# Kernel optimization log

Hardware: AMD Instinct MI355X
Metric: run time of the kernel (lower is better)

## Reference

```python
import jax, jax.numpy as jnp
import numpy as np

BS, SEQ, D_SSL = 256, 201, 1024
D1, D2 = 128, 64
N_NODE = SEQ // 3          # 67 nodes after max_pool1d(3)
N_POOL = int(N_NODE * 0.8) # 53 nodes after GraphPool(k=0.8)
EPS = 1e-5                 # BatchNorm eps (eval mode, running stats)


def setup_inputs() -> dict:
    key = jax.random.key(0)
    ks = jax.random.split(key, 16)
    def rn(k, shape, s=0.02):
        return jax.random.normal(k, shape, jnp.float32) * s
    return {
        "feat": jax.random.normal(ks[0], (BS, SEQ, D_SSL), jnp.float32),
        "W_ll": rn(ks[1], (D_SSL, D1)), "b_ll": jnp.zeros((D1,), jnp.float32),
        "bn1_g": jnp.ones((D1,), jnp.float32), "bn1_b": jnp.zeros((D1,), jnp.float32),
        "bn1_m": rn(ks[2], (D1,), 0.1),
        "bn1_v": jax.random.uniform(ks[3], (D1,), jnp.float32, 0.5, 1.5),
        "W_ap": rn(ks[4], (D1, D2)), "b_ap": jnp.zeros((D2,), jnp.float32),
        "att_w": rn(ks[5], (D2, 1), 0.1),
        "W_pa": rn(ks[6], (D1, D2)), "b_pa": jnp.zeros((D2,), jnp.float32),
        "W_pn": rn(ks[7], (D1, D2)), "b_pn": jnp.zeros((D2,), jnp.float32),
        "bn2_g": jnp.ones((D2,), jnp.float32), "bn2_b": jnp.zeros((D2,), jnp.float32),
        "bn2_m": rn(ks[8], (D2,), 0.1),
        "bn2_v": jax.random.uniform(ks[9], (D2,), jnp.float32, 0.5, 1.5),
        "W_pool": rn(ks[10], (D2, 1), 0.1), "b_pool": jnp.zeros((1,), jnp.float32),
        "W_proj": rn(ks[11], (D2, 1), 0.1), "b_proj": jnp.zeros((1,), jnp.float32),
        "W_node": rn(ks[12], (N_POOL, 2), 0.1), "b_node": jnp.zeros((2,), jnp.float32),
    }


def _bn(x, g, b, m, v):
    # eval-mode BatchNorm1d with running stats, applied per-channel (last dim)
    return (x - m) * jax.lax.rsqrt(v + EPS) * g + b


def reference(feat, W_ll, b_ll, bn1_g, bn1_b, bn1_m, bn1_v,
              W_ap, b_ap, att_w, W_pa, b_pa, W_pn, b_pn,
              bn2_g, bn2_b, bn2_m, bn2_v,
              W_pool, b_pool, W_proj, b_proj, W_node, b_node):
    # LL: (bs, seq, 1024) -> (bs, seq, 128)
    x = feat @ W_ll + b_ll
    # max_pool1d(kernel=3, stride=3) over the sequence dim -> (bs, 67, 128)
    x = x[:, :N_NODE * 3].reshape(BS, N_NODE, 3, D1).max(axis=2)
    x = jax.nn.selu(_bn(x, bn1_g, bn1_b, bn1_m, bn1_v))
    # --- GraphAttentionLayer ---
    pair = x[:, :, None, :] * x[:, None, :, :]            # (bs, n, n, 128) pairwise mul
    att = jnp.tanh(pair @ W_ap + b_ap) @ att_w            # (bs, n, n, 1)
    att = jax.nn.softmax(att, axis=-2)                    # softmax over second node axis
    x1 = jnp.einsum('bij,bjd->bid', att[..., 0], x) @ W_pa + b_pa
    x2 = x @ W_pn + b_pn
    h = jax.nn.selu(_bn(x1 + x2, bn2_g, bn2_b, bn2_m, bn2_v))  # (bs, n, 64)
    # --- GraphPool: top-k node selection ---
    scores = jax.nn.sigmoid(h @ W_pool + b_pool)          # (bs, n, 1)
    _, idx = jax.lax.top_k(scores[..., 0], N_POOL)        # (bs, 53)
    hs = jnp.take_along_axis(h * scores, idx[:, :, None], axis=1)  # (bs, 53, 64)
    # head: proj -> (bs, 53), proj_node -> (bs, 2)
    out = (hs @ W_proj + b_proj)[..., 0] @ W_node + b_node
    return out
```

## Files before the change

### kernel.cpp

```cpp
#include <hip/hip_runtime.h>
#include <stdint.h>
#include <math.h>


#define BS 256
#define SEQ 201
#define DS 1024
#define D1 128
#define D2 64
#define NN 67
#define NP 53
#define ROWS1 (BS * SEQ)
#define ROWS2 (BS * NN)

#define SELU_LAM 1.0507009873554805f
#define SELU_ALP 1.6732632423543772f

__device__ __forceinline__ float selu_f(float x) {
    return (x > 0.0f) ? SELU_LAM * x : SELU_LAM * (SELU_ALP * expm1f(x));
}

__device__ __forceinline__ float fc(float4 v, int k) {
    switch (k & 3) {
        case 0: return v.x;
        case 1: return v.y;
        case 2: return v.z;
        default: return v.w;
    }
}

__global__ __launch_bounds__(256) void k_pre(
    const float* __restrict__ Wll, const float* __restrict__ Wap,
    const float* __restrict__ v1, const float* __restrict__ v2,
    float* __restrict__ WllT, float* __restrict__ WapT,
    float* __restrict__ r1, float* __restrict__ r2)
{
    int t = blockIdx.x * 256 + threadIdx.x;
    if (t < 131072) {
        int c = t >> 10, k = t & 1023;
        WllT[t] = Wll[k * D1 + c];
    } else if (t < 139264) {
        int i = t - 131072; int c = i >> 7, d = i & 127;
        WapT[i] = Wap[d * D2 + c];
    } else if (t < 139392) {
        int d = t - 139264;
        r1[d] = 1.0f / sqrtf(v1[d] + 1e-5f);
    } else if (t < 139456) {
        int c = t - 139392;
        r2[c] = 1.0f / sqrtf(v2[c] + 1e-5f);
    }
}

__global__ __launch_bounds__(256) void k_gemm1(
    const float* __restrict__ A, const float* __restrict__ Bt,
    float* __restrict__ y)
{
    __shared__ __align__(16) float As[128 * 36];
    __shared__ __align__(16) float Bs[128 * 36];
    int tid = threadIdx.x;
    int row0 = blockIdx.x * 128;
    int ty = tid >> 4, tx = tid & 15;
    float acc[8][8];
#pragma unroll
    for (int r = 0; r < 8; ++r)
#pragma unroll
        for (int m = 0; m < 8; ++m) acc[r][m] = 0.0f;

    int lr = tid >> 1, lc = (tid & 1) * 16;
    const float* gA = A + (size_t)(row0 + lr) * DS + lc;
    const float* gB = Bt + (size_t)lr * DS + lc;
    float* wa = As + lr * 36 + lc;
    float* wb = Bs + lr * 36 + lc;

    for (int k0 = 0; k0 < DS; k0 += 32) {
        float4 a0 = *(const float4*)(gA + k0);
        float4 a1 = *(const float4*)(gA + k0 + 4);
        float4 a2 = *(const float4*)(gA + k0 + 8);
        float4 a3 = *(const float4*)(gA + k0 + 12);
        float4 b0 = *(const float4*)(gB + k0);
        float4 b1 = *(const float4*)(gB + k0 + 4);
        float4 b2 = *(const float4*)(gB + k0 + 8);
        float4 b3 = *(const float4*)(gB + k0 + 12);
        __syncthreads();
        *(float4*)(wa)      = a0; *(float4*)(wa + 4)  = a1;
        *(float4*)(wa + 8)  = a2; *(float4*)(wa + 12) = a3;
        *(float4*)(wb)      = b0; *(float4*)(wb + 4)  = b1;
        *(float4*)(wb + 8)  = b2; *(float4*)(wb + 12) = b3;
        __syncthreads();
#pragma unroll
        for (int k4 = 0; k4 < 8; ++k4) {
            float4 av[8], bv[8];
#pragma unroll
            for (int r = 0; r < 8; ++r)
                av[r] = *(const float4*)(As + (ty + 16 * r) * 36 + k4 * 4);
#pragma unroll
            for (int m = 0; m < 8; ++m)
                bv[m] = *(const float4*)(Bs + (tx + 16 * m) * 36 + k4 * 4);
#pragma unroll
            for (int r = 0; r < 8; ++r)
#pragma unroll
                for (int m = 0; m < 8; ++m) {
                    acc[r][m] += av[r].x * bv[m].x;
                    acc[r][m] += av[r].y * bv[m].y;
                    acc[r][m] += av[r].z * bv[m].z;
                    acc[r][m] += av[r].w * bv[m].w;
                }
        }
    }
#pragma unroll
    for (int r = 0; r < 8; ++r)
#pragma unroll
        for (int m = 0; m < 8; ++m)
            y[(size_t)(row0 + ty + 16 * r) * D1 + tx + 16 * m] = acc[r][m];
}

__global__ __launch_bounds__(256) void k_pool(
    const float* __restrict__ y, const float* __restrict__ bll,
    const float* __restrict__ g1, const float* __restrict__ b1,
    const float* __restrict__ m1, const float* __restrict__ r1,
    float* __restrict__ X)
{
    int t = blockIdx.x * 256 + threadIdx.x;
    int d = t & 127, rem = t >> 7;
    int n = rem % NN, b = rem / NN;
    size_t base = ((size_t)(b * SEQ + 3 * n)) * D1 + d;
    float bl = bll[d];
    float v0 = y[base] + bl;
    float v1v = y[base + D1] + bl;
    float v2v = y[base + 2 * D1] + bl;
    float v = fmaxf(fmaxf(v0, v1v), v2v);
    v = (v - m1[d]) * r1[d] * g1[d] + b1[d];
    X[(size_t)rem * D1 + d] = selu_f(v);
}

__global__ __launch_bounds__(256) void k_attn1(
    const float* __restrict__ X, const float* __restrict__ WapT,
    const float* __restrict__ bap, const float* __restrict__ attw,
    float* __restrict__ epart)
{
    __shared__ __align__(16) float Xs[80 * 132];
    int tid = threadIdx.x;
    int blk = blockIdx.x;
    int b = blk >> 1, z = blk & 1;
    const float* Xb = X + (size_t)b * NN * D1;

#pragma unroll
    for (int q = 0; q < 40; ++q) {
        int t = q * 256 + tid;
        int r = t >> 7, d = t & 127;
        Xs[r * 132 + d] = (r < NN) ? Xb[(size_t)r * D1 + d] : 0.0f;
    }
    __syncthreads();

    int ti = tid >> 4, tj = tid & 15;

    float eacc[5][5];
#pragma unroll
    for (int a = 0; a < 5; ++a)
#pragma unroll
        for (int m = a; m < 5; ++m) eacc[a][m] = 0.0f;

    for (int cg = z * 8; cg < z * 8 + 8; ++cg) {
        float E[5][5][4];
#pragma unroll
        for (int a = 0; a < 5; ++a)
#pragma unroll
            for (int m = a; m < 5; ++m)
#pragma unroll
                for (int c = 0; c < 4; ++c) E[a][m][c] = 0.0f;

#pragma unroll 2
        for (int k4 = 0; k4 < 32; ++k4) {
            float4 xa[5], xv[5], w[4];
#pragma unroll
            for (int a = 0; a < 5; ++a)
                xa[a] = *(const float4*)(Xs + (ti + 16 * a) * 132 + k4 * 4);
#pragma unroll
            for (int m = 0; m < 5; ++m)
                xv[m] = *(const float4*)(Xs + (tj + 16 * m) * 132 + k4 * 4);
#pragma unroll
            for (int c = 0; c < 4; ++c)
                w[c] = *(const float4*)(WapT + (cg * 4 + c) * D1 + k4 * 4);
#pragma unroll
            for (int kk = 0; kk < 4; ++kk) {
#pragma unroll
                for (int a = 0; a < 5; ++a) {
                    float pa = fc(xa[a], kk);
#pragma unroll
                    for (int m = a; m < 5; ++m) {
                        float P = pa * fc(xv[m], kk);
                        E[a][m][0] += P * fc(w[0], kk);
                        E[a][m][1] += P * fc(w[1], kk);
                        E[a][m][2] += P * fc(w[2], kk);
                        E[a][m][3] += P * fc(w[3], kk);
                    }
                }
            }
        }
#pragma unroll
        for (int c = 0; c < 4; ++c) {
            float bc = bap[cg * 4 + c], ac = attw[cg * 4 + c];
#pragma unroll
            for (int a = 0; a < 5; ++a)
#pragma unroll
                for (int m = a; m < 5; ++m)
                    eacc[a][m] += tanhf(E[a][m][c] + bc) * ac;
        }
    }

    float* ep = epart + (size_t)blk * 6400;
#pragma unroll
    for (int a = 0; a < 5; ++a)
#pragma unroll
        for (int m = a; m < 5; ++m) {
            int i = ti + 16 * a, j = tj + 16 * m;
            ep[i * 80 + j] = eacc[a][m];
            if (a < m) ep[j * 80 + i] = eacc[a][m];
        }
}

__global__ __launch_bounds__(256) void k_attn2(
    const float* __restrict__ X, const float* __restrict__ epart,
    float* __restrict__ XA)
{
    __shared__ __align__(16) float Xs[80 * 132];
    __shared__ float e[80 * 85];
    int tid = threadIdx.x;
    int b = blockIdx.x;
    const float* Xb = X + (size_t)b * NN * D1;

#pragma unroll
    for (int q = 0; q < 40; ++q) {
        int t = q * 256 + tid;
        int r = t >> 7, d = t & 127;
        Xs[r * 132 + d] = (r < NN) ? Xb[(size_t)r * D1 + d] : 0.0f;
    }
    const float* e0 = epart + (size_t)(b * 2) * 6400;
    const float* e1 = e0 + 6400;
    for (int t = tid; t < 6400; t += 256) {
        int i = t / 80, j = t - i * 80;
        e[i * 85 + j] = e0[t] + e1[t];
    }
    __syncthreads();

    if (tid < NN) {
        float* er = e + tid * 85;
        float mx = -1e30f;
        for (int j = 0; j < NN; ++j) mx = fmaxf(mx, er[j]);
        float sum = 0.0f;
        for (int j = 0; j < NN; ++j) { float p = expf(er[j] - mx); er[j] = p; sum += p; }
        float inv = 1.0f / sum;
        for (int j = 0; j < NN; ++j) er[j] *= inv;
    }
    __syncthreads();

    int ti = tid >> 4, tj = tid & 15;
    int d0 = tj * 8;
    float o[5][8];
#pragma unroll
    for (int a = 0; a < 5; ++a)
#pragma unroll
        for (int dd = 0; dd < 8; ++dd) o[a][dd] = 0.0f;
    for (int j = 0; j < NN; ++j) {
        float4 x0 = *(const float4*)(Xs + j * 132 + d0);
        float4 x1 = *(const float4*)(Xs + j * 132 + d0 + 4);
        float av[5];
#pragma unroll
        for (int a = 0; a < 5; ++a) av[a] = e[(ti + 16 * a) * 85 + j];
#pragma unroll
        for (int a = 0; a < 5; ++a) {
            o[a][0] += av[a] * x0.x; o[a][1] += av[a] * x0.y;
            o[a][2] += av[a] * x0.z; o[a][3] += av[a] * x0.w;
            o[a][4] += av[a] * x1.x; o[a][5] += av[a] * x1.y;
            o[a][6] += av[a] * x1.z; o[a][7] += av[a] * x1.w;
        }
    }
#pragma unroll
    for (int a = 0; a < 5; ++a) {
        int i = ti + 16 * a;
        if (i < NN) {
            float* dst = XA + (size_t)(b * NN + i) * D1 + d0;
            float4 s0, s1;
            s0.x = o[a][0]; s0.y = o[a][1]; s0.z = o[a][2]; s0.w = o[a][3];
            s1.x = o[a][4]; s1.y = o[a][5]; s1.z = o[a][6]; s1.w = o[a][7];
            *(float4*)(dst) = s0;
            *(float4*)(dst + 4) = s1;
        }
    }
}

__global__ __launch_bounds__(256) void k_gemm2(
    const float* __restrict__ XAg, const float* __restrict__ Xg,
    const float* __restrict__ Wpa, const float* __restrict__ Wpn,
    const float* __restrict__ bpa, const float* __restrict__ bpn,
    const float* __restrict__ g2, const float* __restrict__ b2,
    const float* __restrict__ m2, const float* __restrict__ r2,
    float* __restrict__ h)
{
    __shared__ __align__(16) float As[64 * 260];
    __shared__ __align__(16) float Ws[256 * 68];
    int tid = threadIdx.x;
    int row0 = blockIdx.x * 64;
#pragma unroll
    for (int q = 0; q < 16; ++q) {
        int e4 = q * 256 + tid;
        int r = e4 >> 6, k4 = (e4 & 63) * 4;
        float4 v;
        if (k4 < 128) v = *(const float4*)(XAg + (size_t)(row0 + r) * D1 + k4);
        else          v = *(const float4*)(Xg + (size_t)(row0 + r) * D1 + (k4 - 128));
        *(float4*)(As + r * 260 + k4) = v;
    }
#pragma unroll
    for (int q = 0; q < 16; ++q) {
        int e4 = q * 256 + tid;
        int k = e4 >> 4, c4 = (e4 & 15) * 4;
        float4 v;
        if (k < 128) v = *(const float4*)(Wpa + k * D2 + c4);
        else         v = *(const float4*)(Wpn + (k - 128) * D2 + c4);
        *(float4*)(Ws + k * 68 + c4) = v;
    }
    __syncthreads();
    int rl = tid >> 2, cq = (tid & 3) * 16;
    float acc[16];
#pragma unroll
    for (int m = 0; m < 16; ++m) acc[m] = 0.0f;
    for (int k = 0; k < 256; ++k) {
        float a = As[rl * 260 + k];
        float4 w0 = *(const float4*)(Ws + k * 68 + cq);
        float4 w1 = *(const float4*)(Ws + k * 68 + cq + 4);
        float4 w2 = *(const float4*)(Ws + k * 68 + cq + 8);
        float4 w3 = *(const float4*)(Ws + k * 68 + cq + 12);
        acc[0] += a * w0.x;  acc[1] += a * w0.y;  acc[2] += a * w0.z;  acc[3] += a * w0.w;
        acc[4] += a * w1.x;  acc[5] += a * w1.y;  acc[6] += a * w1.z;  acc[7] += a * w1.w;
        acc[8] += a * w2.x;  acc[9] += a * w2.y;  acc[10] += a * w2.z; acc[11] += a * w2.w;
        acc[12] += a * w3.x; acc[13] += a * w3.y; acc[14] += a * w3.z; acc[15] += a * w3.w;
    }
#pragma unroll
    for (int m = 0; m < 16; ++m) {
        int c = cq + m;
        float t = acc[m] + bpa[c] + bpn[c];
        t = (t - m2[c]) * r2[c] * g2[c] + b2[c];
        h[(size_t)(row0 + rl) * D2 + c] = selu_f(t);
    }
}

__global__ __launch_bounds__(64) void k_head(
    const float* __restrict__ h, const float* __restrict__ Wpool,
    const float* __restrict__ bpool, const float* __restrict__ Wproj,
    const float* __restrict__ bproj, const float* __restrict__ Wnode,
    const float* __restrict__ bnode, float* __restrict__ out)
{
    __shared__ float sc[NN], pv[NN], sel[NP];
    int lane = threadIdx.x, b = blockIdx.x;
    for (int j = lane; j < NN; j += 64) {
        const float* hr = h + (size_t)(b * NN + j) * D2;
        float z = 0.0f;
        for (int c = 0; c < D2; ++c) z += hr[c] * Wpool[c];
        z += bpool[0];
        float s = 1.0f / (1.0f + expf(-z));
        float q = 0.0f;
        for (int c = 0; c < D2; ++c) q += (hr[c] * s) * Wproj[c];
        q += bproj[0];
        sc[j] = s; pv[j] = q;
    }
    __syncthreads();
    for (int j = lane; j < NN; j += 64) {
        float sj = sc[j]; int rank = 0;
        for (int k = 0; k < NN; ++k) {
            float sk = sc[k];
            rank += (sk > sj) || (sk == sj && k < j);
        }
        if (rank < NP) sel[rank] = pv[j];
    }
    __syncthreads();
    if (lane < 2) {
        float o = 0.0f;
        for (int r = 0; r < NP; ++r) o += sel[r] * Wnode[r * 2 + lane];
        out[b * 2 + lane] = o + bnode[lane];
    }
}

extern "C" void kernel_launch(void* const* d_in, const int* in_sizes, int n_in,
                              void* d_out, int out_size, void* d_ws, size_t ws_size,
                              hipStream_t stream)
{
    const float* feat  = (const float*)d_in[0];
    const float* Wll   = (const float*)d_in[1];
    const float* bll   = (const float*)d_in[2];
    const float* g1    = (const float*)d_in[3];
    const float* b1    = (const float*)d_in[4];
    const float* m1    = (const float*)d_in[5];
    const float* v1    = (const float*)d_in[6];
    const float* Wap   = (const float*)d_in[7];
    const float* bap   = (const float*)d_in[8];
    const float* attw  = (const float*)d_in[9];
    const float* Wpa   = (const float*)d_in[10];
    const float* bpa   = (const float*)d_in[11];
    const float* Wpn   = (const float*)d_in[12];
    const float* bpn   = (const float*)d_in[13];
    const float* g2    = (const float*)d_in[14];
    const float* b2    = (const float*)d_in[15];
    const float* m2    = (const float*)d_in[16];
    const float* v2    = (const float*)d_in[17];
    const float* Wpool = (const float*)d_in[18];
    const float* bpool = (const float*)d_in[19];
    const float* Wproj = (const float*)d_in[20];
    const float* bproj = (const float*)d_in[21];
    const float* Wnode = (const float*)d_in[22];
    const float* bnode = (const float*)d_in[23];
    float* out = (float*)d_out;

    char* w = (char*)d_ws;
    float* y    = (float*)w; w += (size_t)ROWS1 * D1 * 4;
    float* X    = (float*)w; w += (size_t)ROWS2 * D1 * 4;
    float* XA   = (float*)w; w += (size_t)ROWS2 * D1 * 4;
    float* hbuf = (float*)w; w += (size_t)ROWS2 * D2 * 4;
    float* WllT = (float*)w; w += (size_t)128 * 1024 * 4;
    float* WapT = (float*)w; w += (size_t)64 * 128 * 4;
    float* r1   = (float*)w; w += 128 * 4;
    float* r2   = (float*)w; w += 64 * 4;
    float* epart = y;

    hipLaunchKernelGGL(k_pre,   dim3(545),  dim3(256), 0, stream,
                       Wll, Wap, v1, v2, WllT, WapT, r1, r2);
    hipLaunchKernelGGL(k_gemm1, dim3(402),  dim3(256), 0, stream, feat, WllT, y);
    hipLaunchKernelGGL(k_pool,  dim3(8576), dim3(256), 0, stream,
                       y, bll, g1, b1, m1, r1, X);
    hipLaunchKernelGGL(k_attn1, dim3(512),  dim3(256), 0, stream,
                       X, WapT, bap, attw, epart);
    hipLaunchKernelGGL(k_attn2, dim3(256),  dim3(256), 0, stream,
                       X, epart, XA);
    hipLaunchKernelGGL(k_gemm2, dim3(268),  dim3(256), 0, stream,
                       XA, X, Wpa, Wpn, bpa, bpn, g2, b2, m2, r2, hbuf);
    hipLaunchKernelGGL(k_head,  dim3(256),  dim3(64),  0, stream,
                       hbuf, Wpool, bpool, Wproj, bproj, Wnode, bnode, out);
}
```

Measured before the change: 810.8 us.

## Split-K the input GEMM, prefetch A tiles, split attention further, stage head in LDS

The first GEMM now splits its K dimension in two across twice as many blocks, writing two partial outputs that the pooling kernel sums, and register-prefetches the next A tile while the current one is computed. The attention score kernel splits its channel groups four ways instead of two, and the softmax kernel sums four partials. The head kernel stages each batch's h rows into padded shared memory before its dot products. These aim to fill more of the GPU's compute units in the launch-bound 402- and 512-block grids, at the cost of an extra partial-output buffer that must be written and read back, and extra register pressure from the prefetch.

```diff
diff --git a/kernel.cpp b/kernel.cpp
--- a/kernel.cpp
+++ b/kernel.cpp
@@ -53,12 +53,22 @@
 
 __global__ __launch_bounds__(256) void k_gemm1(
     const float* __restrict__ A, const float* __restrict__ Bt,
-    float* __restrict__ y)
+    float* __restrict__ y0, float* __restrict__ y1, int nsplit)
 {
     __shared__ __align__(16) float As[128 * 36];
     __shared__ __align__(16) float Bs[128 * 36];
     int tid = threadIdx.x;
-    int row0 = blockIdx.x * 128;
+    int bx = blockIdx.x;
+    int tile, kb, nk;
+    float* yout;
+    if (nsplit == 2) {
+        tile = bx >> 1; int half = bx & 1;
+        kb = half << 9; nk = 512;
+        yout = half ? y1 : y0;
+    } else {
+        tile = bx; kb = 0; nk = 1024; yout = y0;
+    }
+    int row0 = tile * 128;
     int ty = tid >> 4, tx = tid & 15;
     float acc[8][8];
 #pragma unroll
@@ -67,26 +77,33 @@
         for (int m = 0; m < 8; ++m) acc[r][m] = 0.0f;
 
     int lr = tid >> 1, lc = (tid & 1) * 16;
-    const float* gA = A + (size_t)(row0 + lr) * DS + lc;
-    const float* gB = Bt + (size_t)lr * DS + lc;
+    const float* gA = A + (size_t)(row0 + lr) * DS + kb + lc;
+    const float* gB = Bt + (size_t)lr * DS + kb + lc;
     float* wa = As + lr * 36 + lc;
     float* wb = Bs + lr * 36 + lc;
 
-    for (int k0 = 0; k0 < DS; k0 += 32) {
-        float4 a0 = *(const float4*)(gA + k0);
-        float4 a1 = *(const float4*)(gA + k0 + 4);
-        float4 a2 = *(const float4*)(gA + k0 + 8);
-        float4 a3 = *(const float4*)(gA + k0 + 12);
+    float4 pa0 = *(const float4*)(gA);
+    float4 pa1 = *(const float4*)(gA + 4);
+    float4 pa2 = *(const float4*)(gA + 8);
+    float4 pa3 = *(const float4*)(gA + 12);
+
+    for (int k0 = 0; k0 < nk; k0 += 32) {
         float4 b0 = *(const float4*)(gB + k0);
         float4 b1 = *(const float4*)(gB + k0 + 4);
         float4 b2 = *(const float4*)(gB + k0 + 8);
         float4 b3 = *(const float4*)(gB + k0 + 12);
         __syncthreads();
-        *(float4*)(wa)      = a0; *(float4*)(wa + 4)  = a1;
-        *(float4*)(wa + 8)  = a2; *(float4*)(wa + 12) = a3;
-        *(float4*)(wb)      = b0; *(float4*)(wb + 4)  = b1;
-        *(float4*)(wb + 8)  = b2; *(float4*)(wb + 12) = b3;
+        *(float4*)(wa)      = pa0; *(float4*)(wa + 4)  = pa1;
+        *(float4*)(wa + 8)  = pa2; *(float4*)(wa + 12) = pa3;
+        *(float4*)(wb)      = b0;  *(float4*)(wb + 4)  = b1;
+        *(float4*)(wb + 8)  = b2;  *(float4*)(wb + 12) = b3;
         __syncthreads();
+        if (k0 + 32 < nk) {
+            pa0 = *(const float4*)(gA + k0 + 32);
+            pa1 = *(const float4*)(gA + k0 + 36);
+            pa2 = *(const float4*)(gA + k0 + 40);
+            pa3 = *(const float4*)(gA + k0 + 44);
+        }
 #pragma unroll
         for (int k4 = 0; k4 < 8; ++k4) {
             float4 av[8], bv[8];
@@ -111,11 +128,12 @@
     for (int r = 0; r < 8; ++r)
 #pragma unroll
         for (int m = 0; m < 8; ++m)
-            y[(size_t)(row0 + ty + 16 * r) * D1 + tx + 16 * m] = acc[r][m];
+            yout[(size_t)(row0 + ty + 16 * r) * D1 + tx + 16 * m] = acc[r][m];
 }
 
 __global__ __launch_bounds__(256) void k_pool(
-    const float* __restrict__ y, const float* __restrict__ bll,
+    const float* __restrict__ y0, const float* __restrict__ y1, int dual,
+    const float* __restrict__ bll,
     const float* __restrict__ g1, const float* __restrict__ b1,
     const float* __restrict__ m1, const float* __restrict__ r1,
     float* __restrict__ X)
@@ -125,10 +143,11 @@
     int n = rem % NN, b = rem / NN;
     size_t base = ((size_t)(b * SEQ + 3 * n)) * D1 + d;
     float bl = bll[d];
-    float v0 = y[base] + bl;
-    float v1v = y[base + D1] + bl;
-    float v2v = y[base + 2 * D1] + bl;
-    float v = fmaxf(fmaxf(v0, v1v), v2v);
+    float s0 = y0[base], s1 = y0[base + D1], s2 = y0[base + 2 * D1];
+    if (dual) {
+        s0 += y1[base]; s1 += y1[base + D1]; s2 += y1[base + 2 * D1];
+    }
+    float v = fmaxf(fmaxf(s0 + bl, s1 + bl), s2 + bl);
     v = (v - m1[d]) * r1[d] * g1[d] + b1[d];
     X[(size_t)rem * D1 + d] = selu_f(v);
 }
@@ -141,7 +160,7 @@
     __shared__ __align__(16) float Xs[80 * 132];
     int tid = threadIdx.x;
     int blk = blockIdx.x;
-    int b = blk >> 1, z = blk & 1;
+    int b = blk >> 2, z = blk & 3;
     const float* Xb = X + (size_t)b * NN * D1;
 
 #pragma unroll
@@ -160,7 +179,7 @@
 #pragma unroll
         for (int m = a; m < 5; ++m) eacc[a][m] = 0.0f;
 
-    for (int cg = z * 8; cg < z * 8 + 8; ++cg) {
+    for (int cg = z * 4; cg < z * 4 + 4; ++cg) {
         float E[5][5][4];
 #pragma unroll
         for (int a = 0; a < 5; ++a)
@@ -235,11 +254,10 @@
         int r = t >> 7, d = t & 127;
         Xs[r * 132 + d] = (r < NN) ? Xb[(size_t)r * D1 + d] : 0.0f;
     }
-    const float* e0 = epart + (size_t)(b * 2) * 6400;
-    const float* e1 = e0 + 6400;
+    const float* e0 = epart + (size_t)(b * 4) * 6400;
     for (int t = tid; t < 6400; t += 256) {
         int i = t / 80, j = t - i * 80;
-        e[i * 85 + j] = e0[t] + e1[t];
+        e[i * 85 + j] = (e0[t] + e0[6400 + t]) + (e0[12800 + t] + e0[19200 + t]);
     }
     __syncthreads();
 
@@ -350,10 +368,19 @@
     const float* __restrict__ bproj, const float* __restrict__ Wnode,
     const float* __restrict__ bnode, float* __restrict__ out)
 {
+    __shared__ float hs[NN * 65];
     __shared__ float sc[NN], pv[NN], sel[NP];
     int lane = threadIdx.x, b = blockIdx.x;
+    const float* hb = h + (size_t)(b * NN) * D2;
+    for (int t = lane; t < NN * 16; t += 64) {
+        int j = t >> 4, c4 = (t & 15) * 4;
+        float4 v = *(const float4*)(hb + (size_t)j * D2 + c4);
+        float* dst = hs + j * 65 + c4;
+        dst[0] = v.x; dst[1] = v.y; dst[2] = v.z; dst[3] = v.w;
+    }
+    __syncthreads();
     for (int j = lane; j < NN; j += 64) {
-        const float* hr = h + (size_t)(b * NN + j) * D2;
+        const float* hr = hs + j * 65;
         float z = 0.0f;
         for (int c = 0; c < D2; ++c) z += hr[c] * Wpool[c];
         z += bpool[0];
@@ -410,23 +437,33 @@
     const float* bnode = (const float*)d_in[23];
     float* out = (float*)d_out;
 
+    const size_t ybytes = (size_t)ROWS1 * D1 * 4;
+    const size_t xbytes = (size_t)ROWS2 * D1 * 4;
+    const size_t hbytes = (size_t)ROWS2 * D2 * 4;
+    const size_t wbytes = (size_t)128 * 1024 * 4 + 64 * 128 * 4 + 4096;
+    size_t need2 = 2 * ybytes + 2 * xbytes + hbytes + wbytes;
+    int nsplit = (ws_size >= need2) ? 2 : 1;
+
     char* w = (char*)d_ws;
-    float* y    = (float*)w; w += (size_t)ROWS1 * D1 * 4;
-    float* X    = (float*)w; w += (size_t)ROWS2 * D1 * 4;
-    float* XA   = (float*)w; w += (size_t)ROWS2 * D1 * 4;
-    float* hbuf = (float*)w; w += (size_t)ROWS2 * D2 * 4;
+    float* y0 = (float*)w; w += ybytes;
+    float* y1 = y0;
+    if (nsplit == 2) { y1 = (float*)w; w += ybytes; }
+    float* X    = (float*)w; w += xbytes;
+    float* XA   = (float*)w; w += xbytes;
+    float* hbuf = (float*)w; w += hbytes;
     float* WllT = (float*)w; w += (size_t)128 * 1024 * 4;
     float* WapT = (float*)w; w += (size_t)64 * 128 * 4;
     float* r1   = (float*)w; w += 128 * 4;
     float* r2   = (float*)w; w += 64 * 4;
-    float* epart = y;
+    float* epart = y0;
 
     hipLaunchKernelGGL(k_pre,   dim3(545),  dim3(256), 0, stream,
                        Wll, Wap, v1, v2, WllT, WapT, r1, r2);
-    hipLaunchKernelGGL(k_gemm1, dim3(402),  dim3(256), 0, stream, feat, WllT, y);
+    hipLaunchKernelGGL(k_gemm1, dim3(nsplit == 2 ? 804 : 402), dim3(256), 0, stream,
+                       feat, WllT, y0, y1, nsplit);
     hipLaunchKernelGGL(k_pool,  dim3(8576), dim3(256), 0, stream,
-                       y, bll, g1, b1, m1, r1, X);
-    hipLaunchKernelGGL(k_attn1, dim3(512),  dim3(256), 0, stream,
+                       y0, y1, nsplit - 1, bll, g1, b1, m1, r1, X);
+    hipLaunchKernelGGL(k_attn1, dim3(1024), dim3(256), 0, stream,
                        X, WapT, bap, attw, epart);
     hipLaunchKernelGGL(k_attn2, dim3(256),  dim3(256), 0, stream,
                        X, epart, XA);
```

Measured after the change: 846.1 us. 4.4% more time.
